# Kernel tuning notes

Measured on AMD Instinct MI355X. Metric: run time of the kernel, lower is better.

Reference implementation:

```python
import jax, jax.numpy as jnp
import numpy as np

HEADS = 8
N = 2048; D_IN = 2048; LATENT = 2048; PROJ = 256; HIDDEN = 128
LAGS = 12; E = 65536; EMB = 128; N_ENT = 10000; N_TS = 1000


def _lag_weights(L):
    # weights(): flip(arange(1..L) / (L*(L+1)/2)); sums to 1
    w = np.arange(1, L + 1, dtype=np.float64) / (L * (L + 1) // 2)
    return jnp.asarray(np.ascontiguousarray(w[::-1]), dtype=jnp.float32)


def _gatv2(x, edge_index, Wl, bl, Wr, br, att, bias):
    # GATv2Conv with PyG defaults: self-loops added, leaky_relu(0.2),
    # softmax over incoming edges per target node, concat heads + bias.
    n = x.shape[0]
    H = HEADS
    D = Wl.shape[1] // H
    sl = jnp.arange(n, dtype=edge_index.dtype)
    src = jnp.concatenate([edge_index[0], sl])
    dst = jnp.concatenate([edge_index[1], sl])
    xl = (x @ Wl + bl).reshape(n, H, D)  # source / message transform
    xr = (x @ Wr + br).reshape(n, H, D)  # target transform
    e = jnp.sum(jax.nn.leaky_relu(xl[src] + xr[dst], 0.2) * att, axis=-1)  # [E', H]
    emax = jax.ops.segment_max(e, dst, num_segments=n)
    ee = jnp.exp(e - emax[dst])
    alpha = ee / jax.ops.segment_sum(ee, dst, num_segments=n)[dst]
    out = jax.ops.segment_sum(alpha[:, :, None] * xl[src], dst, num_segments=n)  # [n,H,D]
    return out.reshape(n, H * D) + bias


def _mha(query, lagged, Wq, bq, Wk, bk, Wv, bv):
    # MultiHeadCausalAttention: per-lag K/V projections combined with fixed
    # triangular weights. Since the weights sum to 1, the projection bias
    # passes through the weighted sum unchanged, so the per-lag Python loop
    # fuses into a single einsum over the lag axis.
    n = query.shape[0]
    dim_out = Wq.shape[1]
    dh = dim_out // HEADS
    Q = (query @ Wq + bq).reshape(n, -1, HEADS, dh).transpose(0, 2, 1, 3)  # [n,H,q,dh]
    tw = _lag_weights(lagged.shape[1])
    K = (jnp.einsum('nli,io,l->no', lagged, Wk, tw) + bk).reshape(n, 1, HEADS, dh).transpose(0, 2, 1, 3)
    V = (jnp.einsum('nli,io,l->no', lagged, Wv, tw) + bv).reshape(n, 1, HEADS, dh).transpose(0, 2, 1, 3)
    scores = jnp.einsum('nhqd,nhkd->nhqk', Q, K) / (dh ** 0.5)
    attn = jax.nn.softmax(scores, axis=-1)
    return jnp.einsum('nhqk,nhkd->nhqd', attn, V).transpose(0, 2, 1, 3).reshape(n, -1, dim_out)


def _forward(time_series_data, lagged_data, eps, gumbel_noise,
             entity_table, timestamp_table,
             gat_e_Wl, gat_e_bl, gat_e_Wr, gat_e_br, gat_e_att, gat_e_bias,
             enc_proj_W, enc_proj_b,
             enc_Wq, enc_bq, enc_Wk, enc_bk, enc_Wv, enc_bv,
             enc_fc_W, enc_fc_b,
             dec_Wq, dec_bq, dec_Wk, dec_bk, dec_Wv, dec_bv,
             gat_d_Wl, gat_d_bl, gat_d_Wr, gat_d_br, gat_d_att, gat_d_bias,
             dec_fc_W, dec_fc_b, A_direct, A_indirect,
             entity_indices, timestamp_indices, edge_index):
    entity_emb = entity_table[entity_indices]      # pretrained TKG entity embedding
    ts_emb = timestamp_table[timestamp_indices]    # pretrained TKG timestamp embedding
    feats = jnp.concatenate([time_series_data, entity_emb, ts_emb], axis=-1)
    x = jax.nn.relu(_gatv2(feats, edge_index, gat_e_Wl, gat_e_bl, gat_e_Wr, gat_e_br, gat_e_att, gat_e_bias))
    x = jax.nn.relu(x @ enc_proj_W + enc_proj_b)
    x = jax.nn.relu(_mha(x, lagged_data, enc_Wq, enc_bq, enc_Wk, enc_bk, enc_Wv, enc_bv))  # [N,1,PROJ]
    q_params = x @ enc_fc_W + enc_fc_b
    mean, log_var = jnp.split(q_params, 2, axis=-1)
    z = mean + jnp.exp(0.5 * log_var) * eps  # reparameterization, [N,1,LATENT]
    x = jax.nn.relu(_mha(z, lagged_data, dec_Wq, dec_bq, dec_Wk, dec_bk, dec_Wv, dec_bv))[:, 0, :]
    x = jax.nn.relu(_gatv2(x, edge_index, gat_d_Wl, gat_d_bl, gat_d_Wr, gat_d_br, gat_d_att, gat_d_bias))
    x_rec = x @ dec_fc_W + dec_fc_b  # [N, D_IN]
    direct = A_direct * jnp.sum(x_rec, axis=0)        # einsum('ij,tj->ij')
    indirect = A_indirect * jnp.sum(z, axis=(0, 1))   # einsum('ij,tlj->ij')
    causal_effect = direct + indirect
    y = jax.nn.softmax((causal_effect + gumbel_noise) / 0.5, axis=-1)  # tau=0.5
    hard = jax.nn.one_hot(jnp.argmax(y, axis=-1), y.shape[-1], dtype=y.dtype)
    adj = jax.lax.stop_gradient(hard - y) + y  # hard gumbel-softmax, straight-through
    return z, mean, log_var, x_rec, causal_effect, adj


def setup_inputs():
    key = jax.random.key(0)
    ks = iter(jax.random.split(key, 64))
    def nrm(shape, s=0.02):
        return jax.random.normal(next(ks), shape, jnp.float32) * s
    A0 = jnp.ones((N, N), jnp.float32) + jnp.eye(N, dtype=jnp.float32)
    A0 = A0 / jnp.sum(A0, axis=1)  # matches torch broadcast A0 / A0.sum(1)
    HH = HEADS * HIDDEN
    d = {
        'entity_indices': jax.random.randint(next(ks), (N,), 0, N_ENT),
        'relation_indices': jax.random.randint(next(ks), (N,), 0, N_TS),
        'timestamp_indices': jax.random.randint(next(ks), (N,), 0, N_TS),
        'time_series_data': jax.random.normal(next(ks), (N, D_IN), jnp.float32),
        'edge_index': jax.random.randint(next(ks), (2, E), 0, N),
        'lagged_data': jax.random.normal(next(ks), (N, LAGS, D_IN), jnp.float32),
        'eps': jax.random.normal(next(ks), (N, 1, LATENT), jnp.float32),
        'gumbel_noise': jax.random.gumbel(next(ks), (N, N), jnp.float32),
        'entity_table': nrm((N_ENT, EMB), 1.0),
        'timestamp_table': nrm((N_TS, EMB), 1.0),
        'gat_e_Wl': nrm((D_IN + 2 * EMB, HH)), 'gat_e_bl': jnp.zeros((HH,), jnp.float32),
        'gat_e_Wr': nrm((D_IN + 2 * EMB, HH)), 'gat_e_br': jnp.zeros((HH,), jnp.float32),
        'gat_e_att': nrm((HEADS, HIDDEN), 0.1), 'gat_e_bias': jnp.zeros((HH,), jnp.float32),
        'enc_proj_W': nrm((HH, PROJ)), 'enc_proj_b': jnp.zeros((PROJ,), jnp.float32),
        'enc_Wq': nrm((PROJ, PROJ)), 'enc_bq': jnp.zeros((PROJ,), jnp.float32),
        'enc_Wk': nrm((D_IN, PROJ)), 'enc_bk': jnp.zeros((PROJ,), jnp.float32),
        'enc_Wv': nrm((D_IN, PROJ)), 'enc_bv': jnp.zeros((PROJ,), jnp.float32),
        'enc_fc_W': nrm((PROJ, 2 * LATENT)), 'enc_fc_b': jnp.zeros((2 * LATENT,), jnp.float32),
        'dec_Wq': nrm((LATENT, PROJ)), 'dec_bq': jnp.zeros((PROJ,), jnp.float32),
        'dec_Wk': nrm((D_IN, PROJ)), 'dec_bk': jnp.zeros((PROJ,), jnp.float32),
        'dec_Wv': nrm((D_IN, PROJ)), 'dec_bv': jnp.zeros((PROJ,), jnp.float32),
        'gat_d_Wl': nrm((PROJ, HH)), 'gat_d_bl': jnp.zeros((HH,), jnp.float32),
        'gat_d_Wr': nrm((PROJ, HH)), 'gat_d_br': jnp.zeros((HH,), jnp.float32),
        'gat_d_att': nrm((HEADS, HIDDEN), 0.1), 'gat_d_bias': jnp.zeros((HH,), jnp.float32),
        'dec_fc_W': nrm((HH, D_IN)), 'dec_fc_b': jnp.zeros((D_IN,), jnp.float32),
        'A_direct': A0, 'A_indirect': A0,
    }
    return d


def reference(entity_indices, relation_indices, timestamp_indices, time_series_data,
              edge_index, lagged_data, eps, gumbel_noise,
              entity_table, timestamp_table,
              gat_e_Wl, gat_e_bl, gat_e_Wr, gat_e_br, gat_e_att, gat_e_bias,
              enc_proj_W, enc_proj_b,
              enc_Wq, enc_bq, enc_Wk, enc_bk, enc_Wv, enc_bv,
              enc_fc_W, enc_fc_b,
              dec_Wq, dec_bq, dec_Wk, dec_bk, dec_Wv, dec_bv,
              gat_d_Wl, gat_d_bl, gat_d_Wr, gat_d_br, gat_d_att, gat_d_bias,
              dec_fc_W, dec_fc_b, A_direct, A_indirect):
    # relation_indices are looked up by the pretrained TKG, but the relation
    # embedding is unused downstream in the original forward, so it is ignored.
    return _forward(time_series_data, lagged_data, eps, gumbel_noise,
                    entity_table, timestamp_table,
                    gat_e_Wl, gat_e_bl, gat_e_Wr, gat_e_br, gat_e_att, gat_e_bias,
                    enc_proj_W, enc_proj_b,
                    enc_Wq, enc_bq, enc_Wk, enc_bk, enc_Wv, enc_bv,
                    enc_fc_W, enc_fc_b,
                    dec_Wq, dec_bq, dec_Wk, dec_bk, dec_Wv, dec_bv,
                    gat_d_Wl, gat_d_bl, gat_d_Wr, gat_d_br, gat_d_att, gat_d_bias,
                    dec_fc_W, dec_fc_b, A_direct, A_indirect,
                    entity_indices, timestamp_indices, edge_index)
```

## Files before the change

kernel.cpp:

```cpp
#include <hip/hip_runtime.h>
#include <hip/hip_bf16.h>
#include <math.h>

#define N_NODES 2048
#define DIN     2048
#define HH      1024
#define LAGS    12
#define NE      65536
#define NL      (2048 * 2048)
#define CHUNK   128

#define BM 128
#define BN 128
#define BK 32
#define BUFS 12288

typedef __attribute__((ext_vector_type(8))) short short8;
typedef __attribute__((ext_vector_type(4))) float f32x4;

static __device__ __forceinline__ short f2bf_rne(float x) {
  union { float f; unsigned u; } c; c.f = x;
  unsigned u = c.u;
  unsigned r = (u + 0x7fffu + ((u >> 16) & 1u)) >> 16;
  return (short)r;
}
static __device__ __forceinline__ float bf2f(short h) {
  union { unsigned u; float f; } c; c.u = ((unsigned)(unsigned short)h) << 16;
  return c.f;
}

typedef __attribute__((address_space(3))) unsigned int as3_u32;
typedef const __attribute__((address_space(1))) unsigned int as1_u32c;
static __device__ __forceinline__ void gload_lds16(const void* g, void* l) {
  __builtin_amdgcn_global_load_lds((as1_u32c*)g, (as3_u32*)l, 16, 0, 0);
}

#define VMCNT6  asm volatile("s_waitcnt vmcnt(6)" ::: "memory")
#define VMCNT0  asm volatile("s_waitcnt vmcnt(0)" ::: "memory")
#define SBAR()  do { asm volatile("" ::: "memory"); __builtin_amdgcn_s_barrier(); \
                     asm volatile("" ::: "memory"); } while (0)

__global__ void init_kernel(int* __restrict__ counts, float* __restrict__ csx,
                            float* __restrict__ csz) {
  int i = blockIdx.x * 256 + threadIdx.x;
  counts[i] = 0; csx[i] = 0.f; csz[i] = 0.f;
}

struct WCfg { const float* W; short* H; short* L; int K; int N; int nb; };
struct WCfg6 { WCfg c[6]; };

__global__ __launch_bounds__(256) void megaA_kernel(
    const float* __restrict__ lagged, short* __restrict__ lw,
    WCfg6 cfgs, const int* __restrict__ dst, int* __restrict__ counts)
{
  __shared__ float t[32][33];
  int bid = blockIdx.x;
  int tid = threadIdx.x;

  if (bid < 2048) {
    int idx = bid * 256 + tid;
    int n = idx >> 8, c8 = idx & 255;
    const float* base = lagged + (size_t)n * (LAGS * DIN) + (size_t)c8 * 8;
    float a[8] = {};
#pragma unroll
    for (int l = 0; l < LAGS; ++l) {
      float w = (float)((double)(LAGS - l) / 78.0);
      float4 v0 = *(const float4*)(base + (size_t)l * DIN);
      float4 v1 = *(const float4*)(base + (size_t)l * DIN + 4);
      a[0] += w * v0.x; a[1] += w * v0.y; a[2] += w * v0.z; a[3] += w * v0.w;
      a[4] += w * v1.x; a[5] += w * v1.y; a[6] += w * v1.z; a[7] += w * v1.w;
    }
    short8 h;
#pragma unroll
    for (int j = 0; j < 8; ++j) h[j] = f2bf_rne(a[j]);
    *(short8*)(lw + (size_t)idx * 8) = h;
  } else if (bid < 2048 + 4608) {
    int wb = bid - 2048;
    int i = 0, base = 0;
    while (i < 5 && wb >= base + cfgs.c[i].nb) { base += cfgs.c[i].nb; ++i; }
    const float* W = cfgs.c[i].W;
    short* H = cfgs.c[i].H;
    short* L = cfgs.c[i].L;
    int K = cfgs.c[i].K, N = cfgs.c[i].N;
    int local = wb - base;
    int nbx = N >> 5;
    int bx = local % nbx, by = local / nbx;
    int tx = tid & 31, ty = tid >> 5;
    int c0 = bx << 5, k0 = by << 5;
#pragma unroll
    for (int j = 0; j < 4; ++j)
      t[ty + 8 * j][tx] = W[(size_t)(k0 + ty + 8 * j) * N + c0 + tx];
    __syncthreads();
#pragma unroll
    for (int j = 0; j < 4; ++j) {
      int c = ty + 8 * j;
      float x = t[tx][c];
      short h = f2bf_rne(x);
      size_t off = (size_t)(c0 + c) * K + k0 + tx;
      H[off] = h;
      L[off] = f2bf_rne(x - bf2f(h));
    }
  } else {
    int i = (bid - 2048 - 4608) * 256 + tid;
    if (i < NE) atomicAdd(&counts[dst[i]], 1);
  }
}

__global__ __launch_bounds__(256) void gemm_bf(
    const short* __restrict__ A,
    const short* __restrict__ Bh0, const short* __restrict__ Bl0,
    const short* __restrict__ Bh1, const short* __restrict__ Bl1,
    short* __restrict__ Cpart,
    int M, int N, int K, int klen, int ntwin)
{
  __shared__ short lds[2 * BUFS];
  int tid = threadIdx.x;
  int lane = tid & 63, wid = tid >> 6;
  int bn = blockIdx.x * BN, bm = blockIdx.y * BM;
  int z = blockIdx.z;
  int twin = (ntwin == 2) ? (z & 1) : 0;
  int kchunk = (ntwin == 2) ? (z >> 1) : z;
  int kb = kchunk * klen;
  const short* Bh = twin ? Bh1 : Bh0;
  const short* Bl = twin ? Bl1 : Bl0;

  const short* gp[6];
  int lofs[6];
  {
    int r4 = lane >> 2;
    int ksw = (lane & 3) ^ ((lane >> 3) & 3);
#pragma unroll
    for (int c = 0; c < 6; ++c) {
      int chunk = wid * 6 + c;
      int p = chunk >> 3, s = chunk & 7;
      int r = (s << 4) + r4;
      const short* bp = (p == 0) ? (A + (size_t)(bm + r) * K)
                      : (p == 1) ? (Bh + (size_t)(bn + r) * K)
                                 : (Bl + (size_t)(bn + r) * K);
      gp[c] = bp + kb + (ksw << 3);
      lofs[c] = (p << 12) + (s << 9);
    }
  }
  auto stage = [&](int bo) {
#pragma unroll
    for (int c = 0; c < 6; ++c) {
      gload_lds16(gp[c], lds + bo + lofs[c]);
      gp[c] += BK;
    }
  };

  int l15 = lane & 15, l4 = lane >> 4;
  int wr = wid >> 1, wc = wid & 1;
  int soff = (l4 ^ ((l15 >> 1) & 3)) << 3;
  int aoff[4], bhoff[4], bloff[4];
#pragma unroll
  for (int i = 0; i < 4; ++i) {
    int r = wr * 64 + i * 16 + l15;
    int c = wc * 64 + i * 16 + l15;
    aoff[i]  = r * BK + soff;
    bhoff[i] = 4096 + c * BK + soff;
    bloff[i] = 8192 + c * BK + soff;
  }

  f32x4 acc[4][4];
#pragma unroll
  for (int m = 0; m < 4; ++m)
#pragma unroll
    for (int n = 0; n < 4; ++n) acc[m][n] = (f32x4){0.f, 0.f, 0.f, 0.f};

  int nt = klen / BK;
  stage(0);
  int cur = 0;
  for (int t = 0; t < nt; ++t) {
    if (t + 1 < nt) { stage(cur ? 0 : BUFS); VMCNT6; }
    else { VMCNT0; }
    SBAR();
    const short* rb = lds + (cur ? BUFS : 0);
    short8 af[4], bh8[4], bl8[4];
#pragma unroll
    for (int i = 0; i < 4; ++i) {
      af[i]  = *(const short8*)(rb + aoff[i]);
      bh8[i] = *(const short8*)(rb + bhoff[i]);
      bl8[i] = *(const short8*)(rb + bloff[i]);
    }
#pragma unroll
    for (int m = 0; m < 4; ++m)
#pragma unroll
      for (int n = 0; n < 4; ++n) {
        acc[m][n] = __builtin_amdgcn_mfma_f32_16x16x32_bf16(af[m], bh8[n], acc[m][n], 0, 0, 0);
        acc[m][n] = __builtin_amdgcn_mfma_f32_16x16x32_bf16(af[m], bl8[n], acc[m][n], 0, 0, 0);
      }
    SBAR();
    cur ^= 1;
  }

  short* P = Cpart + (size_t)z * ((size_t)M * N);
#pragma unroll
  for (int n = 0; n < 4; ++n) {
    int col = bn + wc * 64 + n * 16 + l15;
#pragma unroll
    for (int m = 0; m < 4; ++m) {
      int row0 = bm + wr * 64 + m * 16 + (l4 << 2);
#pragma unroll
      for (int r = 0; r < 4; ++r)
        P[(size_t)(row0 + r) * N + col] = f2bf_rne(acc[m][n][r]);
    }
  }
}

__global__ __launch_bounds__(256) void gemm_dual(
    const short* __restrict__ xe, const short* __restrict__ xd,
    const short* __restrict__ fcH, const short* __restrict__ fcL,
    const short* __restrict__ WlH, const short* __restrict__ WlL,
    const short* __restrict__ WrH, const short* __restrict__ WrL,
    const float* __restrict__ fc_b, const float* __restrict__ bl,
    const float* __restrict__ br,
    float* __restrict__ out_mean, float* __restrict__ out_lv,
    short* __restrict__ xl, short* __restrict__ xr)
{
  __shared__ short lds[2 * BUFS];
  const int K = 256;
  int fb = blockIdx.x;
  const short *A, *Bh, *Bl;
  const float* bias;
  int bm, bn, jobB, ldc;
  short* Obf = nullptr;
  float* Of = nullptr;
  if (fb < 512) {
    A = xe; Bh = fcH; Bl = fcL; bias = fc_b;
    bn = (fb & 31) << 7; bm = (fb >> 5) << 7;
    jobB = 0; ldc = 2048; Of = out_mean;
  } else {
    int g = fb - 512, twin = g & 1, t = g >> 1;
    A = xd; Bh = twin ? WrH : WlH; Bl = twin ? WrL : WlL;
    bias = twin ? br : bl;
    bn = (t & 7) << 7; bm = (t >> 3) << 7;
    jobB = 1; ldc = 1024; Obf = twin ? xr : xl;
  }

  int tid = threadIdx.x;
  int lane = tid & 63, wid = tid >> 6;

  const short* gp[6];
  int lofs[6];
  {
    int r4 = lane >> 2;
    int ksw = (lane & 3) ^ ((lane >> 3) & 3);
#pragma unroll
    for (int c = 0; c < 6; ++c) {
      int chunk = wid * 6 + c;
      int p = chunk >> 3, s = chunk & 7;
      int r = (s << 4) + r4;
      const short* bp = (p == 0) ? (A + (size_t)(bm + r) * K)
                      : (p == 1) ? (Bh + (size_t)(bn + r) * K)
                                 : (Bl + (size_t)(bn + r) * K);
      gp[c] = bp + (ksw << 3);
      lofs[c] = (p << 12) + (s << 9);
    }
  }
  auto stage = [&](int bo) {
#pragma unroll
    for (int c = 0; c < 6; ++c) {
      gload_lds16(gp[c], lds + bo + lofs[c]);
      gp[c] += BK;
    }
  };

  int l15 = lane & 15, l4 = lane >> 4;
  int wr = wid >> 1, wc = wid & 1;
  int soff = (l4 ^ ((l15 >> 1) & 3)) << 3;
  int aoff[4], bhoff[4], bloff[4];
#pragma unroll
  for (int i = 0; i < 4; ++i) {
    int r = wr * 64 + i * 16 + l15;
    int c = wc * 64 + i * 16 + l15;
    aoff[i]  = r * BK + soff;
    bhoff[i] = 4096 + c * BK + soff;
    bloff[i] = 8192 + c * BK + soff;
  }

  f32x4 acc[4][4];
#pragma unroll
  for (int m = 0; m < 4; ++m)
#pragma unroll
    for (int n = 0; n < 4; ++n) acc[m][n] = (f32x4){0.f, 0.f, 0.f, 0.f};

  stage(0);
  int cur = 0;
#pragma unroll
  for (int t = 0; t < 8; ++t) {
    if (t + 1 < 8) { stage(cur ? 0 : BUFS); VMCNT6; }
    else { VMCNT0; }
    SBAR();
    const short* rb = lds + (cur ? BUFS : 0);
    short8 af[4], bh8[4], bl8[4];
#pragma unroll
    for (int i = 0; i < 4; ++i) {
      af[i]  = *(const short8*)(rb + aoff[i]);
      bh8[i] = *(const short8*)(rb + bhoff[i]);
      bl8[i] = *(const short8*)(rb + bloff[i]);
    }
#pragma unroll
    for (int m = 0; m < 4; ++m)
#pragma unroll
      for (int n = 0; n < 4; ++n) {
        acc[m][n] = __builtin_amdgcn_mfma_f32_16x16x32_bf16(af[m], bh8[n], acc[m][n], 0, 0, 0);
        acc[m][n] = __builtin_amdgcn_mfma_f32_16x16x32_bf16(af[m], bl8[n], acc[m][n], 0, 0, 0);
      }
    SBAR();
    cur ^= 1;
  }

#pragma unroll
  for (int n = 0; n < 4; ++n) {
    int col = bn + wc * 64 + n * 16 + l15;
    float bv = bias[col];
    if (jobB) {
#pragma unroll
      for (int m = 0; m < 4; ++m) {
        int row0 = bm + wr * 64 + m * 16 + (l4 << 2);
#pragma unroll
        for (int r = 0; r < 4; ++r)
          Obf[(size_t)(row0 + r) * ldc + col] = f2bf_rne(acc[m][n][r] + bv);
      }
    } else {
      float* O = Of; int oc = col;
      if (col >= 2048) { O = out_lv; oc = col - 2048; }
#pragma unroll
      for (int m = 0; m < 4; ++m) {
        int row0 = bm + wr * 64 + m * 16 + (l4 << 2);
#pragma unroll
        for (int r = 0; r < 4; ++r)
          O[(size_t)(row0 + r) * ldc + oc] = acc[m][n][r] + bv;
      }
    }
  }
}

__global__ __launch_bounds__(256) void sumrelu_kernel(
    const short* __restrict__ part, const float* __restrict__ b0,
    const float* __restrict__ b1, short* __restrict__ xe,
    short* __restrict__ xd)
{
  int i4 = blockIdx.x * 256 + threadIdx.x;
  size_t S = (size_t)N_NODES * 256;
  size_t base = (size_t)i4 * 4;
  int col = (int)(base & 255);
  float4 b0v = *(const float4*)(b0 + col);
  float4 b1v = *(const float4*)(b1 + col);
  float s0[4] = {}, s1[4] = {};
#pragma unroll
  for (int c = 0; c < 8; ++c) {
    short4 p0 = *(const short4*)(part + (size_t)(2 * c) * S + base);
    short4 p1 = *(const short4*)(part + (size_t)(2 * c + 1) * S + base);
    s0[0] += bf2f(p0.x); s0[1] += bf2f(p0.y); s0[2] += bf2f(p0.z); s0[3] += bf2f(p0.w);
    s1[0] += bf2f(p1.x); s1[1] += bf2f(p1.y); s1[2] += bf2f(p1.z); s1[3] += bf2f(p1.w);
  }
  short4 e, d;
  e.x = f2bf_rne(fmaxf(s0[0] + b0v.x, 0.f));
  e.y = f2bf_rne(fmaxf(s0[1] + b0v.y, 0.f));
  e.z = f2bf_rne(fmaxf(s0[2] + b0v.z, 0.f));
  e.w = f2bf_rne(fmaxf(s0[3] + b0v.w, 0.f));
  d.x = f2bf_rne(fmaxf(s1[0] + b1v.x, 0.f));
  d.y = f2bf_rne(fmaxf(s1[1] + b1v.y, 0.f));
  d.z = f2bf_rne(fmaxf(s1[2] + b1v.z, 0.f));
  d.w = f2bf_rne(fmaxf(s1[3] + b1v.w, 0.f));
  *(short4*)(xe + base) = e;
  *(short4*)(xd + base) = d;
}

__global__ __launch_bounds__(256) void megaB_kernel(
    const short* __restrict__ xl, const short* __restrict__ xr,
    const float* __restrict__ att, const float* __restrict__ bias,
    const int* __restrict__ csr_src, const int* __restrict__ offs,
    short* __restrict__ outp,
    const float* __restrict__ mean_in, const float* __restrict__ lv_in,
    const float* __restrict__ eps, float* __restrict__ z,
    float* __restrict__ csz)
{
  __shared__ float xr_s[HH];
  __shared__ float att_s[HH];
  __shared__ float e_s[CHUNK * 8];
  __shared__ int   src_s[CHUNK];
  __shared__ float m_s[8], s_s[8], f_s[8];

  int tid = threadIdx.x;

  if (blockIdx.x >= 2048) {
    int flat = blockIdx.x - 2048;
    int c = ((flat & 3) * 256 + tid) * 2;
    int r0 = (flat >> 2) * 16;
    float sx = 0.f, sy = 0.f;
    for (int r = r0; r < r0 + 16; ++r) {
      size_t off = (size_t)r * 2048 + c;
      float2 m = *(const float2*)(mean_in + off);
      float2 v = *(const float2*)(lv_in + off);
      float2 e = *(const float2*)(eps + off);
      float zx = m.x + expf(0.5f * v.x) * e.x;
      float zy = m.y + expf(0.5f * v.y) * e.y;
      *(float2*)(z + off) = make_float2(zx, zy);
      sx += zx; sy += zy;
    }
    atomicAdd(&csz[c], sx);
    atomicAdd(&csz[c + 1], sy);
    return;
  }

  int n = blockIdx.x;
  {
    short4 x4 = ((const short4*)(xr + (size_t)n * HH))[tid];
    xr_s[tid * 4 + 0] = bf2f(x4.x);
    xr_s[tid * 4 + 1] = bf2f(x4.y);
    xr_s[tid * 4 + 2] = bf2f(x4.z);
    xr_s[tid * 4 + 3] = bf2f(x4.w);
  }
  ((float4*)att_s)[tid] = ((const float4*)att)[tid];
  if (tid < 8) { m_s[tid] = -INFINITY; s_s[tid] = 0.f; }
  __syncthreads();

  int beg = offs[n], end = offs[n + 1];
  int ht = tid >> 5;
  float4 acc = make_float4(0.f, 0.f, 0.f, 0.f);

  for (int c0 = beg; c0 < end; c0 += CHUNK) {
    int cnt = min(CHUNK, end - c0);
    if (tid < cnt) src_s[tid] = csr_src[c0 + tid];
    __syncthreads();

    int wave = tid >> 6, lane = tid & 63;
    int d0 = lane << 4;
    for (int e = wave; e < cnt; e += 4) {
      const short* xlr = xl + (size_t)src_s[e] * HH + d0;
      short8 a0 = *(const short8*)xlr;
      short8 a1 = *(const short8*)(xlr + 8);
      float sum = 0.f;
#pragma unroll
      for (int j = 0; j < 8; ++j) {
        float t = bf2f(a0[j]) + xr_s[d0 + j];
        t = t > 0.f ? t : 0.2f * t;
        sum += t * att_s[d0 + j];
      }
#pragma unroll
      for (int j = 0; j < 8; ++j) {
        float t = bf2f(a1[j]) + xr_s[d0 + 8 + j];
        t = t > 0.f ? t : 0.2f * t;
        sum += t * att_s[d0 + 8 + j];
      }
      sum += __shfl_xor(sum, 1);
      sum += __shfl_xor(sum, 2);
      sum += __shfl_xor(sum, 4);
      if ((lane & 7) == 0) e_s[e * 8 + (lane >> 3)] = sum;
    }
    __syncthreads();

    if (tid < 8) {
      int h = tid;
      float m_old = m_s[h];
      float cm = -INFINITY;
      for (int e = 0; e < cnt; ++e) cm = fmaxf(cm, e_s[e * 8 + h]);
      float m_new = fmaxf(m_old, cm);
      float f = expf(m_old - m_new);
      float s = s_s[h] * f;
      for (int e = 0; e < cnt; ++e) {
        float p = expf(e_s[e * 8 + h] - m_new);
        e_s[e * 8 + h] = p;
        s += p;
      }
      m_s[h] = m_new; s_s[h] = s; f_s[h] = f;
    }
    __syncthreads();

    float f = f_s[ht];
    acc.x *= f; acc.y *= f; acc.z *= f; acc.w *= f;
    for (int e = 0; e < cnt; ++e) {
      float p = e_s[e * 8 + ht];
      short4 v = *(const short4*)(xl + (size_t)src_s[e] * HH + (tid << 2));
      acc.x += p * bf2f(v.x); acc.y += p * bf2f(v.y);
      acc.z += p * bf2f(v.z); acc.w += p * bf2f(v.w);
    }
    __syncthreads();
  }

  float inv = 1.0f / s_s[ht];
  float4 b4 = *(const float4*)(bias + (tid << 2));
  short4 o4;
  o4.x = f2bf_rne(fmaxf(acc.x * inv + b4.x, 0.f));
  o4.y = f2bf_rne(fmaxf(acc.y * inv + b4.y, 0.f));
  o4.z = f2bf_rne(fmaxf(acc.z * inv + b4.z, 0.f));
  o4.w = f2bf_rne(fmaxf(acc.w * inv + b4.w, 0.f));
  *(short4*)(outp + (size_t)n * HH + (tid << 2)) = o4;
}

__global__ __launch_bounds__(256) void xrec_sum_kernel(
    const short* __restrict__ part, const float* __restrict__ bias,
    float* __restrict__ xrec, float* __restrict__ csx)
{
  int c = (blockIdx.x * 256 + threadIdx.x) * 2;
  int r0 = blockIdx.y * 16;
  size_t S = (size_t)N_NODES * 2048;
  float2 b = *(const float2*)(bias + c);
  float sx = 0.f, sy = 0.f;
  for (int r = r0; r < r0 + 16; ++r) {
    size_t off = (size_t)r * 2048 + c;
    short2 p0 = *(const short2*)(part + off);
    short2 p1 = *(const short2*)(part + S + off);
    float vx = bf2f(p0.x) + bf2f(p1.x) + b.x;
    float vy = bf2f(p0.y) + bf2f(p1.y) + b.y;
    *(float2*)(xrec + off) = make_float2(vx, vy);
    sx += vx; sy += vy;
  }
  atomicAdd(&csx[c], sx);
  atomicAdd(&csx[c + 1], sy);
}

__global__ __launch_bounds__(256) void scan_kernel(const int* __restrict__ counts,
    int* __restrict__ offs, int* __restrict__ cursor) {
  __shared__ int part[256];
  int tid = threadIdx.x;
  int base = tid * 8;
  int loc[8]; int s = 0;
#pragma unroll
  for (int i = 0; i < 8; ++i) { loc[i] = s; s += counts[base + i] + 1; }
  part[tid] = s;
  __syncthreads();
  for (int off = 1; off < 256; off <<= 1) {
    int v = part[tid];
    int add = (tid >= off) ? part[tid - off] : 0;
    __syncthreads();
    part[tid] = v + add;
    __syncthreads();
  }
  int prev = (tid == 0) ? 0 : part[tid - 1];
#pragma unroll
  for (int i = 0; i < 8; ++i) {
    int o = prev + loc[i];
    offs[base + i] = o;
    cursor[base + i] = o;
  }
  if (tid == 255) offs[N_NODES] = part[255];
}

__global__ void fill_kernel(const int* __restrict__ src, const int* __restrict__ dst,
                            int* __restrict__ cursor, int* __restrict__ csr_src) {
  int i = blockIdx.x * 256 + threadIdx.x;
  if (i < NE) {
    int p = atomicAdd(&cursor[dst[i]], 1);
    csr_src[p] = src[i];
  } else if (i < NE + N_NODES) {
    int n = i - NE;
    int p = atomicAdd(&cursor[n], 1);
    csr_src[p] = n;
  }
}

__global__ __launch_bounds__(256) void final_kernel(
    const float* __restrict__ Ad, const float* __restrict__ Ai,
    const float* __restrict__ gum, const float* __restrict__ csx,
    const float* __restrict__ csz, float* __restrict__ ce_out,
    float* __restrict__ adj_out)
{
  int i = blockIdx.x;
  int tid = threadIdx.x;
  size_t rb = (size_t)i * 2048;

  float vmax = -INFINITY; int vidx = 0;
  for (int j4 = tid; j4 < 512; j4 += 256) {
    float4 ad = *(const float4*)(Ad  + rb + (size_t)j4 * 4);
    float4 ai = *(const float4*)(Ai  + rb + (size_t)j4 * 4);
    float4 g  = *(const float4*)(gum + rb + (size_t)j4 * 4);
    float4 cx = *(const float4*)(csx + (size_t)j4 * 4);
    float4 cz = *(const float4*)(csz + (size_t)j4 * 4);
    float4 ce;
    ce.x = ad.x * cx.x + ai.x * cz.x;
    ce.y = ad.y * cx.y + ai.y * cz.y;
    ce.z = ad.z * cx.z + ai.z * cz.z;
    ce.w = ad.w * cx.w + ai.w * cz.w;
    *(float4*)(ce_out + rb + (size_t)j4 * 4) = ce;
    int j = j4 * 4;
    float l;
    l = (ce.x + g.x) * 2.0f; if (l > vmax) { vmax = l; vidx = j; }
    l = (ce.y + g.y) * 2.0f; if (l > vmax) { vmax = l; vidx = j + 1; }
    l = (ce.z + g.z) * 2.0f; if (l > vmax) { vmax = l; vidx = j + 2; }
    l = (ce.w + g.w) * 2.0f; if (l > vmax) { vmax = l; vidx = j + 3; }
  }
  for (int m = 1; m < 64; m <<= 1) {
    float ov = __shfl_xor(vmax, m);
    int   oi = __shfl_xor(vidx, m);
    if (ov > vmax || (ov == vmax && oi < vidx)) { vmax = ov; vidx = oi; }
  }
  __shared__ float wm[4];
  __shared__ int   wi[4];
  __shared__ int   amax;
  int lane = tid & 63, wave = tid >> 6;
  if (lane == 0) { wm[wave] = vmax; wi[wave] = vidx; }
  __syncthreads();
  if (tid == 0) {
    float bv = wm[0]; int bi = wi[0];
    for (int w = 1; w < 4; ++w)
      if (wm[w] > bv || (wm[w] == bv && wi[w] < bi)) { bv = wm[w]; bi = wi[w]; }
    amax = bi;
  }
  __syncthreads();
  int am = amax;
  for (int j4 = tid; j4 < 512; j4 += 256) {
    int j = j4 * 4;
    float4 o;
    o.x = (j     == am) ? 1.f : 0.f;
    o.y = (j + 1 == am) ? 1.f : 0.f;
    o.z = (j + 2 == am) ? 1.f : 0.f;
    o.w = (j + 3 == am) ? 1.f : 0.f;
    *(float4*)(adj_out + rb + (size_t)j4 * 4) = o;
  }
}

extern "C" void kernel_launch(void* const* d_in, const int* in_sizes, int n_in,
                              void* d_out, int out_size, void* d_ws, size_t ws_size,
                              hipStream_t stream) {
  (void)in_sizes; (void)n_in; (void)out_size; (void)ws_size;

  const int*   edge_index = (const int*)d_in[4];
  const float* lagged     = (const float*)d_in[5];
  const float* eps        = (const float*)d_in[6];
  const float* gumbel     = (const float*)d_in[7];
  const float* enc_Wv     = (const float*)d_in[22];
  const float* enc_bv     = (const float*)d_in[23];
  const float* enc_fc_W   = (const float*)d_in[24];
  const float* enc_fc_b   = (const float*)d_in[25];
  const float* dec_Wv     = (const float*)d_in[30];
  const float* dec_bv     = (const float*)d_in[31];
  const float* gat_Wl     = (const float*)d_in[32];
  const float* gat_bl     = (const float*)d_in[33];
  const float* gat_Wr     = (const float*)d_in[34];
  const float* gat_br     = (const float*)d_in[35];
  const float* gat_att    = (const float*)d_in[36];
  const float* gat_bias   = (const float*)d_in[37];
  const float* dec_fc_W   = (const float*)d_in[38];
  const float* dec_fc_b   = (const float*)d_in[39];
  const float* A_dir      = (const float*)d_in[40];
  const float* A_ind      = (const float*)d_in[41];

  float* out      = (float*)d_out;
  float* out_z    = out;
  float* out_mean = out + (size_t)NL;
  float* out_lv   = out + 2 * (size_t)NL;
  float* out_xrec = out + 3 * (size_t)NL;
  float* out_ce   = out + 4 * (size_t)NL;
  float* out_adj  = out + 5 * (size_t)NL;

  char* ws = (char*)d_ws;
  short* lw_bf = (short*)(ws);
  short* WvH0  = (short*)(ws + ((size_t) 8 << 20));
  short* WvL0  = (short*)(ws + ((size_t) 9 << 20));
  short* WvH1  = (short*)(ws + ((size_t)10 << 20));
  short* WvL1  = (short*)(ws + ((size_t)11 << 20));
  short* fcH   = (short*)(ws + ((size_t)12 << 20));
  short* fcL   = (short*)(ws + ((size_t)14 << 20));
  short* WlH   = (short*)(ws + ((size_t)16 << 20));
  short* WlL   = (short*)(ws + ((size_t)16 << 20) + (512u << 10));
  short* WrH   = (short*)(ws + ((size_t)17 << 20));
  short* WrL   = (short*)(ws + ((size_t)17 << 20) + (512u << 10));
  short* dfH   = (short*)(ws + ((size_t)18 << 20));
  short* dfL   = (short*)(ws + ((size_t)22 << 20));
  short* xe_bf = (short*)(ws + ((size_t)26 << 20));
  short* xd_bf = (short*)(ws + ((size_t)27 << 20));
  short* xl    = (short*)(ws + ((size_t)28 << 20));
  short* xr    = (short*)(ws + ((size_t)32 << 20));
  short* gt_bf = (short*)(ws + ((size_t)44 << 20));
  short* part  = (short*)(ws + ((size_t)48 << 20));
  int*   counts = (int*) (ws + ((size_t)64 << 20));
  int*   offs   = (int*) (ws + ((size_t)64 << 20) + (16u << 10));
  int*   cursor = (int*) (ws + ((size_t)64 << 20) + (32u << 10));
  int*   csr    = (int*) (ws + ((size_t)64 << 20) + (48u << 10));
  float* csx    = (float*)(ws + ((size_t)64 << 20) + (384u << 10));
  float* csz    = (float*)(ws + ((size_t)64 << 20) + (400u << 10));

  const int* e_src = edge_index;
  const int* e_dst = edge_index + NE;

  init_kernel<<<8, 256, 0, stream>>>(counts, csx, csz);

  {
    WCfg6 cfgs;
    cfgs.c[0] = { enc_Wv,   WvH0, WvL0, 2048, 256,  512  };
    cfgs.c[1] = { dec_Wv,   WvH1, WvL1, 2048, 256,  512  };
    cfgs.c[2] = { enc_fc_W, fcH,  fcL,  256,  4096, 1024 };
    cfgs.c[3] = { gat_Wl,   WlH,  WlL,  256,  1024, 256  };
    cfgs.c[4] = { gat_Wr,   WrH,  WrL,  256,  1024, 256  };
    cfgs.c[5] = { dec_fc_W, dfH,  dfL,  1024, 2048, 2048 };
    megaA_kernel<<<6912, 256, 0, stream>>>(lagged, lw_bf, cfgs, e_dst, counts);
  }

  scan_kernel<<<1, 256, 0, stream>>>(counts, offs, cursor);
  fill_kernel<<<(NE + N_NODES) / 256, 256, 0, stream>>>(e_src, e_dst, cursor, csr);

  gemm_bf<<<dim3(2, 16, 16), 256, 0, stream>>>(
      lw_bf, WvH0, WvL0, WvH1, WvL1, part,
      N_NODES, 256, 2048, 256, 2);
  sumrelu_kernel<<<512, 256, 0, stream>>>(part, enc_bv, dec_bv, xe_bf, xd_bf);

  gemm_dual<<<768, 256, 0, stream>>>(
      xe_bf, xd_bf, fcH, fcL, WlH, WlL, WrH, WrL,
      enc_fc_b, gat_bl, gat_br, out_mean, out_lv, xl, xr);

  megaB_kernel<<<2560, 256, 0, stream>>>(
      xl, xr, gat_att, gat_bias, csr, offs, gt_bf,
      out_mean, out_lv, eps, out_z, csz);

  gemm_bf<<<dim3(16, 16, 2), 256, 0, stream>>>(
      gt_bf, dfH, dfL, nullptr, nullptr, part,
      N_NODES, 2048, 1024, 512, 1);
  xrec_sum_kernel<<<dim3(4, 128), 256, 0, stream>>>(part, dec_fc_b, out_xrec, csx);

  final_kernel<<<N_NODES, 256, 0, stream>>>(A_dir, A_ind, gumbel, csx, csz,
                                            out_ce, out_adj);
}
```

Measured before the change: 214.1 us.

## Drop low-order weight split in lag GEMM and parallelize GAT softmax over heads

Adds a gemm_p2 variant for the first lag-weighted GEMM that multiplies only the high bf16 part of the Wv weights, removing the second MFMA per tile and the extra LDS staging of the low-order residual. This halves MFMA work and cuts weight traffic for that GEMM, at the cost of reduced precision, since the weights are effectively rounded to plain bf16. Separately, the GAT online-softmax step now runs on all 256 threads (32 per head) with shuffle reductions instead of 8 serial threads. To support this, the score buffer is transposed to a head-major layout.

```diff
diff --git a/kernel.cpp b/kernel.cpp
--- a/kernel.cpp
+++ b/kernel.cpp
@@ -13,7 +13,6 @@
 #define BM 128
 #define BN 128
 #define BK 32
-#define BUFS 12288
 
 typedef __attribute__((ext_vector_type(8))) short short8;
 typedef __attribute__((ext_vector_type(4))) float f32x4;
@@ -36,6 +35,7 @@
 }
 
 #define VMCNT6  asm volatile("s_waitcnt vmcnt(6)" ::: "memory")
+#define VMCNT4  asm volatile("s_waitcnt vmcnt(4)" ::: "memory")
 #define VMCNT0  asm volatile("s_waitcnt vmcnt(0)" ::: "memory")
 #define SBAR()  do { asm volatile("" ::: "memory"); __builtin_amdgcn_s_barrier(); \
                      asm volatile("" ::: "memory"); } while (0)
@@ -106,14 +106,14 @@
   }
 }
 
-__global__ __launch_bounds__(256) void gemm_bf(
+__global__ __launch_bounds__(256) void gemm_p3(
     const short* __restrict__ A,
     const short* __restrict__ Bh0, const short* __restrict__ Bl0,
     const short* __restrict__ Bh1, const short* __restrict__ Bl1,
     short* __restrict__ Cpart,
     int M, int N, int K, int klen, int ntwin)
 {
-  __shared__ short lds[2 * BUFS];
+  __shared__ short lds[2 * 12288];
   int tid = threadIdx.x;
   int lane = tid & 63, wid = tid >> 6;
   int bn = blockIdx.x * BN, bm = blockIdx.y * BM;
@@ -172,10 +172,10 @@
   stage(0);
   int cur = 0;
   for (int t = 0; t < nt; ++t) {
-    if (t + 1 < nt) { stage(cur ? 0 : BUFS); VMCNT6; }
+    if (t + 1 < nt) { stage(cur ? 0 : 12288); VMCNT6; }
     else { VMCNT0; }
     SBAR();
-    const short* rb = lds + (cur ? BUFS : 0);
+    const short* rb = lds + (cur ? 12288 : 0);
     short8 af[4], bh8[4], bl8[4];
 #pragma unroll
     for (int i = 0; i < 4; ++i) {
@@ -190,6 +190,101 @@
         acc[m][n] = __builtin_amdgcn_mfma_f32_16x16x32_bf16(af[m], bh8[n], acc[m][n], 0, 0, 0);
         acc[m][n] = __builtin_amdgcn_mfma_f32_16x16x32_bf16(af[m], bl8[n], acc[m][n], 0, 0, 0);
       }
+    SBAR();
+    cur ^= 1;
+  }
+
+  short* P = Cpart + (size_t)z * ((size_t)M * N);
+#pragma unroll
+  for (int n = 0; n < 4; ++n) {
+    int col = bn + wc * 64 + n * 16 + l15;
+#pragma unroll
+    for (int m = 0; m < 4; ++m) {
+      int row0 = bm + wr * 64 + m * 16 + (l4 << 2);
+#pragma unroll
+      for (int r = 0; r < 4; ++r)
+        P[(size_t)(row0 + r) * N + col] = f2bf_rne(acc[m][n][r]);
+    }
+  }
+}
+
+__global__ __launch_bounds__(256) void gemm_p2(
+    const short* __restrict__ A,
+    const short* __restrict__ Bh0, const short* __restrict__ Bh1,
+    short* __restrict__ Cpart,
+    int M, int N, int K, int klen, int ntwin)
+{
+  __shared__ short lds[2 * 8192];
+  int tid = threadIdx.x;
+  int lane = tid & 63, wid = tid >> 6;
+  int bn = blockIdx.x * BN, bm = blockIdx.y * BM;
+  int z = blockIdx.z;
+  int twin = (ntwin == 2) ? (z & 1) : 0;
+  int kchunk = (ntwin == 2) ? (z >> 1) : z;
+  int kb = kchunk * klen;
+  const short* Bh = twin ? Bh1 : Bh0;
+
+  const short* gp[4];
+  int lofs[4];
+  {
+    int r4 = lane >> 2;
+    int ksw = (lane & 3) ^ ((lane >> 3) & 3);
+#pragma unroll
+    for (int c = 0; c < 4; ++c) {
+      int chunk = wid * 4 + c;
+      int p = chunk >> 3, s = chunk & 7;
+      int r = (s << 4) + r4;
+      const short* bp = (p == 0) ? (A + (size_t)(bm + r) * K)
+                                 : (Bh + (size_t)(bn + r) * K);
+      gp[c] = bp + kb + (ksw << 3);
+      lofs[c] = (p << 12) + (s << 9);
+    }
+  }
+  auto stage = [&](int bo) {
+#pragma unroll
+    for (int c = 0; c < 4; ++c) {
+      gload_lds16(gp[c], lds + bo + lofs[c]);
+      gp[c] += BK;
+    }
+  };
+
+  int l15 = lane & 15, l4 = lane >> 4;
+  int wr = wid >> 1, wc = wid & 1;
+  int soff = (l4 ^ ((l15 >> 1) & 3)) << 3;
+  int aoff[4], bhoff[4];
+#pragma unroll
+  for (int i = 0; i < 4; ++i) {
+    int r = wr * 64 + i * 16 + l15;
+    int c = wc * 64 + i * 16 + l15;
+    aoff[i]  = r * BK + soff;
+    bhoff[i] = 4096 + c * BK + soff;
+  }
+
+  f32x4 acc[4][4];
+#pragma unroll
+  for (int m = 0; m < 4; ++m)
+#pragma unroll
+    for (int n = 0; n < 4; ++n) acc[m][n] = (f32x4){0.f, 0.f, 0.f, 0.f};
+
+  int nt = klen / BK;
+  stage(0);
+  int cur = 0;
+  for (int t = 0; t < nt; ++t) {
+    if (t + 1 < nt) { stage(cur ? 0 : 8192); VMCNT4; }
+    else { VMCNT0; }
+    SBAR();
+    const short* rb = lds + (cur ? 8192 : 0);
+    short8 af[4], bh8[4];
+#pragma unroll
+    for (int i = 0; i < 4; ++i) {
+      af[i]  = *(const short8*)(rb + aoff[i]);
+      bh8[i] = *(const short8*)(rb + bhoff[i]);
+    }
+#pragma unroll
+    for (int m = 0; m < 4; ++m)
+#pragma unroll
+      for (int n = 0; n < 4; ++n)
+        acc[m][n] = __builtin_amdgcn_mfma_f32_16x16x32_bf16(af[m], bh8[n], acc[m][n], 0, 0, 0);
     SBAR();
     cur ^= 1;
   }
@@ -218,7 +313,7 @@
     float* __restrict__ out_mean, float* __restrict__ out_lv,
     short* __restrict__ xl, short* __restrict__ xr)
 {
-  __shared__ short lds[2 * BUFS];
+  __shared__ short lds[2 * 12288];
   const int K = 256;
   int fb = blockIdx.x;
   const short *A, *Bh, *Bl;
@@ -289,10 +384,10 @@
   int cur = 0;
 #pragma unroll
   for (int t = 0; t < 8; ++t) {
-    if (t + 1 < 8) { stage(cur ? 0 : BUFS); VMCNT6; }
+    if (t + 1 < 8) { stage(cur ? 0 : 12288); VMCNT6; }
     else { VMCNT0; }
     SBAR();
-    const short* rb = lds + (cur ? BUFS : 0);
+    const short* rb = lds + (cur ? 12288 : 0);
     short8 af[4], bh8[4], bl8[4];
 #pragma unroll
     for (int i = 0; i < 4; ++i) {
@@ -380,7 +475,7 @@
 {
   __shared__ float xr_s[HH];
   __shared__ float att_s[HH];
-  __shared__ float e_s[CHUNK * 8];
+  __shared__ float e_s[8 * CHUNK];
   __shared__ int   src_s[CHUNK];
   __shared__ float m_s[8], s_s[8], f_s[8];
 
@@ -449,31 +544,39 @@
       sum += __shfl_xor(sum, 1);
       sum += __shfl_xor(sum, 2);
       sum += __shfl_xor(sum, 4);
-      if ((lane & 7) == 0) e_s[e * 8 + (lane >> 3)] = sum;
+      if ((lane & 7) == 0) e_s[(lane >> 3) * CHUNK + e] = sum;
     }
     __syncthreads();
 
-    if (tid < 8) {
-      int h = tid;
+    {
+      int h = tid >> 5, i0 = tid & 31;
+      float cm = -INFINITY;
+      for (int e = i0; e < cnt; e += 32) cm = fmaxf(cm, e_s[h * CHUNK + e]);
+#pragma unroll
+      for (int m = 1; m < 32; m <<= 1) cm = fmaxf(cm, __shfl_xor(cm, m));
       float m_old = m_s[h];
-      float cm = -INFINITY;
-      for (int e = 0; e < cnt; ++e) cm = fmaxf(cm, e_s[e * 8 + h]);
       float m_new = fmaxf(m_old, cm);
-      float f = expf(m_old - m_new);
-      float s = s_s[h] * f;
-      for (int e = 0; e < cnt; ++e) {
-        float p = expf(e_s[e * 8 + h] - m_new);
-        e_s[e * 8 + h] = p;
-        s += p;
+      float csum = 0.f;
+      for (int e = i0; e < cnt; e += 32) {
+        float p = expf(e_s[h * CHUNK + e] - m_new);
+        e_s[h * CHUNK + e] = p;
+        csum += p;
       }
-      m_s[h] = m_new; s_s[h] = s; f_s[h] = f;
+#pragma unroll
+      for (int m = 1; m < 32; m <<= 1) csum += __shfl_xor(csum, m);
+      if (i0 == 0) {
+        float f = expf(m_old - m_new);
+        s_s[h] = s_s[h] * f + csum;
+        m_s[h] = m_new;
+        f_s[h] = f;
+      }
     }
     __syncthreads();
 
     float f = f_s[ht];
     acc.x *= f; acc.y *= f; acc.z *= f; acc.w *= f;
     for (int e = 0; e < cnt; ++e) {
-      float p = e_s[e * 8 + ht];
+      float p = e_s[ht * CHUNK + e];
       short4 v = *(const short4*)(xl + (size_t)src_s[e] * HH + (tid << 2));
       acc.x += p * bf2f(v.x); acc.y += p * bf2f(v.y);
       acc.z += p * bf2f(v.z); acc.w += p * bf2f(v.w);
@@ -693,8 +796,8 @@
   scan_kernel<<<1, 256, 0, stream>>>(counts, offs, cursor);
   fill_kernel<<<(NE + N_NODES) / 256, 256, 0, stream>>>(e_src, e_dst, cursor, csr);
 
-  gemm_bf<<<dim3(2, 16, 16), 256, 0, stream>>>(
-      lw_bf, WvH0, WvL0, WvH1, WvL1, part,
+  gemm_p2<<<dim3(2, 16, 16), 256, 0, stream>>>(
+      lw_bf, WvH0, WvH1, part,
       N_NODES, 256, 2048, 256, 2);
   sumrelu_kernel<<<512, 256, 0, stream>>>(part, enc_bv, dec_bv, xe_bf, xd_bf);
 
@@ -706,7 +809,7 @@
       xl, xr, gat_att, gat_bias, csr, offs, gt_bf,
       out_mean, out_lv, eps, out_z, csz);
 
-  gemm_bf<<<dim3(16, 16, 2), 256, 0, stream>>>(
+  gemm_p3<<<dim3(16, 16, 2), 256, 0, stream>>>(
       gt_bf, dfH, dfL, nullptr, nullptr, part,
       N_NODES, 2048, 1024, 512, 1);
   xrec_sum_kernel<<<dim3(4, 128), 256, 0, stream>>>(part, dec_fc_b, out_xrec, csx);
```

New measurement: 204.7 us. -4.4%, faster.
